# Optimization experiments

Hardware: AMD Instinct MI355X
Metric: run time of the kernel (lower is better)

The kernel has to match this reference:

```python
import jax, jax.numpy as jnp
import numpy as np

QB = 127.0  # 2**(8-1) - 1
LN_EPS = 1e-5


def _bitlinear(x, W):
    # LayerNorm (no affine)
    mu = jnp.mean(x, axis=-1, keepdims=True)
    var = jnp.mean((x - mu) ** 2, axis=-1, keepdims=True)
    xn = (x - mu) * jax.lax.rsqrt(var + LN_EPS)
    # per-tensor absmax activation fake-quant with STE
    eps = jnp.finfo(x.dtype).eps
    gamma = jnp.maximum(jnp.max(jnp.abs(xn)), 1e-8)
    xs = xn * (QB / gamma)
    xq_hard = jnp.round(jnp.clip(xs, -QB + eps, QB - eps))
    xq = xn + jax.lax.stop_gradient(xq_hard - xn)
    # binary weight quant: sign(W - mean(W)) with STE, scale beta = mean(|W|)
    alpha = jnp.mean(W)
    beta = jnp.maximum(jnp.mean(jnp.abs(W)), 1e-8)
    ws = W - alpha
    wb = ws + jax.lax.stop_gradient(jnp.where(ws > 0, 1.0, -1.0).astype(W.dtype) - ws)
    out = xq @ wb.T  # [B, out_features]
    return out * (beta * gamma / QB)


def setup_inputs() -> dict:
    key = jax.random.key(0)
    k0, k1, k2, k3 = jax.random.split(key, 4)
    B, D_IN, D_H, D_OUT = 131072, 256, 256, 256
    x = jax.random.normal(k0, (B, D_IN), dtype=jnp.float32)
    W1 = jax.random.normal(k1, (D_H, D_IN), dtype=jnp.float32) * 0.02
    W2 = jax.random.normal(k2, (D_H, D_H), dtype=jnp.float32) * 0.02
    W3 = jax.random.normal(k3, (D_OUT, D_H), dtype=jnp.float32) * 0.02
    return {"x": x, "W1": W1, "W2": W2, "W3": W3}


def reference(x, W1, W2, W3):
    h = jax.nn.relu(_bitlinear(x, W1))
    h = jax.nn.relu(_bitlinear(h, W2))
    return _bitlinear(h, W3)
```

## Files before the change

kernel.cpp:

```cpp
#include <hip/hip_runtime.h>
#include <stdint.h>

#define NROWS 131072
#define DIM 256

typedef __attribute__((ext_vector_type(4))) float f32x4;
typedef __attribute__((ext_vector_type(8))) float f32x8;
typedef __attribute__((ext_vector_type(8))) __bf16 bf16x8;
typedef __attribute__((ext_vector_type(8))) short s16x8;

__device__ __forceinline__ short bftrunc(float f) {
  return (short)(__float_as_uint(f) >> 16);
}

__global__ __launch_bounds__(256) void k_stats(const float* __restrict__ x,
                                               float* __restrict__ mu_o, float* __restrict__ rs_o,
                                               unsigned* __restrict__ gslot) {
  const int l = threadIdx.x & 63;
  const int gw = blockIdx.x * 4 + (threadIdx.x >> 6);
  float gmax = 0.f;
  for (int i = 0; i < 16; ++i) {
    const int row = gw * 16 + i;
    f32x4 v = *(const f32x4*)(x + (size_t)row * DIM + l * 4);
    float s = v.x + v.y + v.z + v.w;
    #pragma unroll
    for (int m = 1; m < 64; m <<= 1) s += __shfl_xor(s, m);
    const float mu = s * (1.f / 256.f);
    float d0 = v.x - mu, d1 = v.y - mu, d2 = v.z - mu, d3 = v.w - mu;
    float sq = d0 * d0 + d1 * d1 + d2 * d2 + d3 * d3;
    float am = fmaxf(fmaxf(fabsf(d0), fabsf(d1)), fmaxf(fabsf(d2), fabsf(d3)));
    #pragma unroll
    for (int m = 1; m < 64; m <<= 1) {
      sq += __shfl_xor(sq, m);
      am = fmaxf(am, __shfl_xor(am, m));
    }
    const float rstd = rsqrtf(sq * (1.f / 256.f) + 1e-5f);
    if (l == 0) { mu_o[row] = mu; rs_o[row] = rstd; }
    gmax = fmaxf(gmax, am * rstd);
  }
  if (l == 0) atomicMax(gslot + (gw & 63), __float_as_uint(gmax));
}

__global__ __launch_bounds__(256) void k_wstats1(const float* __restrict__ W0,
                                                 const float* __restrict__ W1,
                                                 const float* __restrict__ W2,
                                                 float2* __restrict__ part) {
  const int layer = blockIdx.y;
  const float* W = layer == 0 ? W0 : (layer == 1 ? W1 : W2);
  const int idx = (blockIdx.x * 256 + threadIdx.x) * 4;
  f32x4 v = *(const f32x4*)(W + idx);
  float s = v.x + v.y + v.z + v.w;
  float sa = fabsf(v.x) + fabsf(v.y) + fabsf(v.z) + fabsf(v.w);
  #pragma unroll
  for (int m = 1; m < 64; m <<= 1) { s += __shfl_xor(s, m); sa += __shfl_xor(sa, m); }
  __shared__ float bs[4], ba[4];
  const int w = threadIdx.x >> 6, l = threadIdx.x & 63;
  if (l == 0) { bs[w] = s; ba[w] = sa; }
  __syncthreads();
  if (threadIdx.x == 0) {
    float2 p;
    p.x = bs[0] + bs[1] + bs[2] + bs[3];
    p.y = ba[0] + ba[1] + ba[2] + ba[3];
    part[layer * 64 + blockIdx.x] = p;
  }
}

__global__ __launch_bounds__(64) void k_wstats2(const float2* __restrict__ part,
                                                float* __restrict__ ab) {
  const int layer = blockIdx.x;
  float2 p = part[layer * 64 + threadIdx.x];
  float s = p.x, sa = p.y;
  #pragma unroll
  for (int m = 1; m < 64; m <<= 1) { s += __shfl_xor(s, m); sa += __shfl_xor(sa, m); }
  if (threadIdx.x == 0) {
    ab[layer] = s * (1.f / 65536.f);
    ab[3 + layer] = fmaxf(sa * (1.f / 65536.f), 1e-8f);
  }
}

__global__ __launch_bounds__(256) void k_pack(const float* __restrict__ W0,
                                              const float* __restrict__ W1,
                                              const float* __restrict__ W2,
                                              const float* __restrict__ ab,
                                              unsigned short* __restrict__ bp) {
  const int layer = blockIdx.y;
  const float* W = layer == 0 ? W0 : (layer == 1 ? W1 : W2);
  const float alpha = ab[layer];
  const int p = blockIdx.x * 256 + threadIdx.x;
  const int r = p & 7, l = (p >> 3) & 63, nt = (p >> 9) & 15, kt = p >> 13;
  const int k = kt * 32 + ((l >> 4) << 3) + r;
  const int j = nt * 16 + (l & 15);
  const float wv = W[j * 256 + k] - alpha;
  bp[layer * 65536 + p] = (wv > 0.f) ? 0x3F80u : 0xBF80u;
}

template <int FINAL>
__global__ __launch_bounds__(256, 2) void k_gemm(
    const float* src, const float* __restrict__ mu, const float* __restrict__ rs,
    const unsigned* __restrict__ gslot, const unsigned short* __restrict__ bp,
    const float* __restrict__ beta_p,
    float* __restrict__ hout, float* bout,
    float* __restrict__ mu_n, float* __restrict__ rs_n, unsigned* __restrict__ gslot_n) {
  const int t = threadIdx.x, l = t & 63, w = t >> 6;
  const int row0 = blockIdx.x * 128 + w * 32;
  const int lr = l & 15, g2 = l >> 4;

  float gm = __uint_as_float(gslot[l]);
  #pragma unroll
  for (int m = 1; m < 64; m <<= 1) gm = fmaxf(gm, __shfl_xor(gm, m));
  const float gamma = fmaxf(gm, 1e-8f);
  const float qs = 127.f / gamma;
  const float beta = *beta_p;
  const float oscale = beta * gamma * (1.f / 127.f);

  const float mu0 = mu[row0 + lr],      rs0 = rs[row0 + lr];
  const float mu1 = mu[row0 + 16 + lr], rs1 = rs[row0 + 16 + lr];

  f32x4 acc[2][16];
  #pragma unroll
  for (int mt = 0; mt < 2; ++mt)
    #pragma unroll
    for (int i = 0; i < 16; ++i) acc[mt][i] = (f32x4){0.f, 0.f, 0.f, 0.f};

  const float* a0p = src + (size_t)(row0 + lr) * DIM + g2 * 8;
  const float* a1p = a0p + 16 * DIM;
  const unsigned short* bpl = bp + l * 8;

  #pragma unroll
  for (int c = 0; c < 8; ++c) {
    f32x8 v0 = *(const f32x8*)(a0p + c * 32);
    f32x8 v1 = *(const f32x8*)(a1p + c * 32);
    union { s16x8 s; bf16x8 b; } a0u, a1u;
    #pragma unroll
    for (int e = 0; e < 8; ++e) {
      float xn = (v0[e] - mu0) * rs0;
      float xs = xn * qs;
      xs = fminf(fmaxf(xs, -127.f), 127.f);
      a0u.s[e] = bftrunc(rintf(xs));
      float yn = (v1[e] - mu1) * rs1;
      float ys = yn * qs;
      ys = fminf(fmaxf(ys, -127.f), 127.f);
      a1u.s[e] = bftrunc(rintf(ys));
    }
    #pragma unroll
    for (int nt = 0; nt < 16; ++nt) {
      bf16x8 b = *(const bf16x8*)(bpl + (c * 16 + nt) * 512);
      acc[0][nt] = __builtin_amdgcn_mfma_f32_16x16x32_bf16(a0u.b, b, acc[0][nt], 0, 0, 0);
      acc[1][nt] = __builtin_amdgcn_mfma_f32_16x16x32_bf16(a1u.b, b, acc[1][nt], 0, 0, 0);
    }
  }

  if constexpr (FINAL == 1) {
    #pragma unroll
    for (int mt = 0; mt < 2; ++mt)
      #pragma unroll
      for (int nt = 0; nt < 16; ++nt)
        #pragma unroll
        for (int rr = 0; rr < 4; ++rr) {
          const int grow = row0 + mt * 16 + g2 * 4 + rr;
          bout[(size_t)grow * DIM + nt * 16 + lr] = acc[mt][nt][rr] * oscale;
        }
  } else {
    float gmax = 0.f;
    #pragma unroll
    for (int mt = 0; mt < 2; ++mt) {
      float sum[4] = {0.f, 0.f, 0.f, 0.f};
      #pragma unroll
      for (int nt = 0; nt < 16; ++nt)
        #pragma unroll
        for (int rr = 0; rr < 4; ++rr) {
          float h = fmaxf(acc[mt][nt][rr] * oscale, 0.f);
          acc[mt][nt][rr] = h;
          sum[rr] += h;
          hout[(size_t)(row0 + mt * 16 + g2 * 4 + rr) * DIM + nt * 16 + lr] = h;
        }
      #pragma unroll
      for (int rr = 0; rr < 4; ++rr) {
        float s_ = sum[rr];
        s_ += __shfl_xor(s_, 1); s_ += __shfl_xor(s_, 2);
        s_ += __shfl_xor(s_, 4); s_ += __shfl_xor(s_, 8);
        const float m_ = s_ * (1.f / 256.f);
        float sq = 0.f, am = 0.f;
        #pragma unroll
        for (int nt = 0; nt < 16; ++nt) {
          float d = acc[mt][nt][rr] - m_;
          sq += d * d;
          am = fmaxf(am, fabsf(d));
        }
        sq += __shfl_xor(sq, 1); sq += __shfl_xor(sq, 2);
        sq += __shfl_xor(sq, 4); sq += __shfl_xor(sq, 8);
        am = fmaxf(am, __shfl_xor(am, 1)); am = fmaxf(am, __shfl_xor(am, 2));
        am = fmaxf(am, __shfl_xor(am, 4)); am = fmaxf(am, __shfl_xor(am, 8));
        const float rstd = rsqrtf(sq * (1.f / 256.f) + 1e-5f);
        const int grow = row0 + mt * 16 + g2 * 4 + rr;
        if (lr == 0) { mu_n[grow] = m_; rs_n[grow] = rstd; }
        gmax = fmaxf(gmax, am * rstd);
      }
    }
    gmax = fmaxf(gmax, __shfl_xor(gmax, 16));
    gmax = fmaxf(gmax, __shfl_xor(gmax, 32));
    if (l == 0) atomicMax(gslot_n + (blockIdx.x & 63), __float_as_uint(gmax));
  }
}

extern "C" void kernel_launch(void* const* d_in, const int* in_sizes, int n_in,
                              void* d_out, int out_size, void* d_ws, size_t ws_size,
                              hipStream_t stream) {
  const float* x  = (const float*)d_in[0];
  const float* W1 = (const float*)d_in[1];
  const float* W2 = (const float*)d_in[2];
  const float* W3 = (const float*)d_in[3];

  char* ws = (char*)d_ws;
  unsigned* gslot = (unsigned*)ws;
  float* ab = (float*)(ws + 1024);
  float2* part = (float2*)(ws + 2048);
  float* muv = (float*)(ws + 4096);
  float* rsv = (float*)(ws + 4096 + 3 * 524288);
  unsigned short* bp = (unsigned short*)(ws + 3149824);
  float* h1 = (float*)(ws + 4194304);
  float* h2 = (float*)d_out;

  hipMemsetAsync(gslot, 0, 768, stream);
  dim3 wg(64, 3);
  k_wstats1<<<wg, 256, 0, stream>>>(W1, W2, W3, part);
  k_wstats2<<<3, 64, 0, stream>>>(part, ab);
  dim3 pg(256, 3);
  k_pack<<<pg, 256, 0, stream>>>(W1, W2, W3, ab, bp);
  k_stats<<<2048, 256, 0, stream>>>(x, muv, rsv, gslot);

  k_gemm<0><<<1024, 256, 0, stream>>>(x, muv, rsv, gslot, bp, ab + 3,
                                      h1, nullptr,
                                      muv + 131072, rsv + 131072, gslot + 64);
  k_gemm<0><<<1024, 256, 0, stream>>>(h1, muv + 131072, rsv + 131072, gslot + 64,
                                      bp + 65536, ab + 4,
                                      h2, nullptr,
                                      muv + 262144, rsv + 262144, gslot + 128);
  k_gemm<1><<<1024, 256, 0, stream>>>(h2, muv + 262144, rsv + 262144, gslot + 128,
                                      bp + 131072, ab + 5,
                                      nullptr, (float*)d_out,
                                      nullptr, nullptr, nullptr);
}
```

Before: 538.7 us.

## Stage A and B tiles through LDS with direct global-to-LDS loads

```diff
diff --git a/kernel.cpp b/kernel.cpp
--- a/kernel.cpp
+++ b/kernel.cpp
@@ -5,12 +5,23 @@
 #define DIM 256
 
 typedef __attribute__((ext_vector_type(4))) float f32x4;
-typedef __attribute__((ext_vector_type(8))) float f32x8;
 typedef __attribute__((ext_vector_type(8))) __bf16 bf16x8;
 typedef __attribute__((ext_vector_type(8))) short s16x8;
 
 __device__ __forceinline__ short bftrunc(float f) {
   return (short)(__float_as_uint(f) >> 16);
+}
+
+__device__ __forceinline__ short quant1(float v, float mu_, float rs_, float qs) {
+  float xn = (v - mu_) * rs_;
+  float xs = xn * qs;
+  xs = fminf(fmaxf(xs, -127.f), 127.f);
+  return bftrunc(rintf(xs));
+}
+
+__device__ __forceinline__ void gload_lds16(const void* g, void* lds) {
+  __builtin_amdgcn_global_load_lds((const __attribute__((address_space(1))) void*)g,
+                                   (__attribute__((address_space(3))) void*)lds, 16, 0, 0);
 }
 
 __global__ __launch_bounds__(256) void k_stats(const float* __restrict__ x,
@@ -95,15 +106,20 @@
 }
 
 template <int FINAL>
-__global__ __launch_bounds__(256, 2) void k_gemm(
+__global__ __launch_bounds__(256, 3) void k_gemm(
     const float* src, const float* __restrict__ mu, const float* __restrict__ rs,
     const unsigned* __restrict__ gslot, const unsigned short* __restrict__ bp,
     const float* __restrict__ beta_p,
     float* __restrict__ hout, float* bout,
     float* __restrict__ mu_n, float* __restrict__ rs_n, unsigned* __restrict__ gslot_n) {
+  __shared__ float Af[4096];
+  __shared__ unsigned short Bb[16384];
+  __shared__ float sS[2][64], sQ[2][64];
+
   const int t = threadIdx.x, l = t & 63, w = t >> 6;
-  const int row0 = blockIdx.x * 128 + w * 32;
   const int lr = l & 15, g2 = l >> 4;
+  const int wr = w >> 1, wc = w & 1;
+  const int row0 = blockIdx.x * 64;
 
   float gm = __uint_as_float(gslot[l]);
   #pragma unroll
@@ -113,92 +129,131 @@
   const float beta = *beta_p;
   const float oscale = beta * gamma * (1.f / 127.f);
 
-  const float mu0 = mu[row0 + lr],      rs0 = rs[row0 + lr];
-  const float mu1 = mu[row0 + 16 + lr], rs1 = rs[row0 + 16 + lr];
-
-  f32x4 acc[2][16];
+  const int arow = wr * 32 + lr;
+  const float mu0 = mu[row0 + arow],      rs0 = rs[row0 + arow];
+  const float mu1 = mu[row0 + arow + 16], rs1 = rs[row0 + arow + 16];
+
+  f32x4 acc[2][8];
   #pragma unroll
   for (int mt = 0; mt < 2; ++mt)
     #pragma unroll
-    for (int i = 0; i < 16; ++i) acc[mt][i] = (f32x4){0.f, 0.f, 0.f, 0.f};
-
-  const float* a0p = src + (size_t)(row0 + lr) * DIM + g2 * 8;
-  const float* a1p = a0p + 16 * DIM;
-  const unsigned short* bpl = bp + l * 8;
-
-  #pragma unroll
-  for (int c = 0; c < 8; ++c) {
-    f32x8 v0 = *(const f32x8*)(a0p + c * 32);
-    f32x8 v1 = *(const f32x8*)(a1p + c * 32);
-    union { s16x8 s; bf16x8 b; } a0u, a1u;
-    #pragma unroll
-    for (int e = 0; e < 8; ++e) {
-      float xn = (v0[e] - mu0) * rs0;
-      float xs = xn * qs;
-      xs = fminf(fmaxf(xs, -127.f), 127.f);
-      a0u.s[e] = bftrunc(rintf(xs));
-      float yn = (v1[e] - mu1) * rs1;
-      float ys = yn * qs;
-      ys = fminf(fmaxf(ys, -127.f), 127.f);
-      a1u.s[e] = bftrunc(rintf(ys));
-    }
-    #pragma unroll
-    for (int nt = 0; nt < 16; ++nt) {
-      bf16x8 b = *(const bf16x8*)(bpl + (c * 16 + nt) * 512);
-      acc[0][nt] = __builtin_amdgcn_mfma_f32_16x16x32_bf16(a0u.b, b, acc[0][nt], 0, 0, 0);
-      acc[1][nt] = __builtin_amdgcn_mfma_f32_16x16x32_bf16(a1u.b, b, acc[1][nt], 0, 0, 0);
-    }
+    for (int i = 0; i < 8; ++i) acc[mt][i] = (f32x4){0.f, 0.f, 0.f, 0.f};
+
+  for (int s = 0; s < 4; ++s) {
+    #pragma unroll
+    for (int it = 0; it < 4; ++it) {
+      const int d = w * 4096 + it * 1024 + l * 16;
+      const int row = d >> 8;
+      const int soff = (d & 255) ^ ((row & 7) << 4);
+      gload_lds16(src + (size_t)(row0 + row) * DIM + s * 64 + (soff >> 2),
+                  (char*)Af + d);
+    }
+    #pragma unroll
+    for (int it = 0; it < 8; ++it) {
+      const int d = w * 8192 + it * 1024 + l * 16;
+      gload_lds16(bp + s * 16384 + (d >> 1), (char*)Bb + d);
+    }
+    __syncthreads();
+
+    #pragma unroll
+    for (int kt2 = 0; kt2 < 2; ++kt2) {
+      bf16x8 af[2];
+      #pragma unroll
+      for (int mt = 0; mt < 2; ++mt) {
+        const int row = wr * 32 + mt * 16 + lr;
+        const int base = row * 256 + kt2 * 128 + g2 * 32;
+        const int sw = (lr & 7) << 4;
+        f32x4 v0 = *(const f32x4*)((const char*)Af + (base ^ sw));
+        f32x4 v1 = *(const f32x4*)((const char*)Af + ((base + 16) ^ sw));
+        const float mu_ = mt ? mu1 : mu0;
+        const float rs_ = mt ? rs1 : rs0;
+        union { s16x8 sv; bf16x8 bv; } u;
+        #pragma unroll
+        for (int e = 0; e < 4; ++e) {
+          u.sv[e]     = quant1(v0[e], mu_, rs_, qs);
+          u.sv[e + 4] = quant1(v1[e], mu_, rs_, qs);
+        }
+        af[mt] = u.bv;
+      }
+      #pragma unroll
+      for (int nt = 0; nt < 8; ++nt) {
+        const int ntg = wc * 8 + nt;
+        bf16x8 b = *(const bf16x8*)&Bb[((kt2 * 16 + ntg) * 64 + l) * 8];
+        acc[0][nt] = __builtin_amdgcn_mfma_f32_16x16x32_bf16(af[0], b, acc[0][nt], 0, 0, 0);
+        acc[1][nt] = __builtin_amdgcn_mfma_f32_16x16x32_bf16(af[1], b, acc[1][nt], 0, 0, 0);
+      }
+    }
+    __syncthreads();
   }
 
   if constexpr (FINAL == 1) {
     #pragma unroll
     for (int mt = 0; mt < 2; ++mt)
       #pragma unroll
-      for (int nt = 0; nt < 16; ++nt)
+      for (int nt = 0; nt < 8; ++nt)
         #pragma unroll
         for (int rr = 0; rr < 4; ++rr) {
-          const int grow = row0 + mt * 16 + g2 * 4 + rr;
-          bout[(size_t)grow * DIM + nt * 16 + lr] = acc[mt][nt][rr] * oscale;
+          const int grow = row0 + wr * 32 + mt * 16 + g2 * 4 + rr;
+          bout[(size_t)grow * DIM + (wc * 8 + nt) * 16 + lr] = acc[mt][nt][rr] * oscale;
         }
   } else {
-    float gmax = 0.f;
+    float ps[2][4], pq[2][4];
     #pragma unroll
     for (int mt = 0; mt < 2; ++mt) {
-      float sum[4] = {0.f, 0.f, 0.f, 0.f};
-      #pragma unroll
-      for (int nt = 0; nt < 16; ++nt)
+      #pragma unroll
+      for (int rr = 0; rr < 4; ++rr) { ps[mt][rr] = 0.f; pq[mt][rr] = 0.f; }
+      #pragma unroll
+      for (int nt = 0; nt < 8; ++nt)
         #pragma unroll
         for (int rr = 0; rr < 4; ++rr) {
           float h = fmaxf(acc[mt][nt][rr] * oscale, 0.f);
           acc[mt][nt][rr] = h;
-          sum[rr] += h;
-          hout[(size_t)(row0 + mt * 16 + g2 * 4 + rr) * DIM + nt * 16 + lr] = h;
+          ps[mt][rr] += h;
+          pq[mt][rr] += h * h;
+          hout[(size_t)(row0 + wr * 32 + mt * 16 + g2 * 4 + rr) * DIM + (wc * 8 + nt) * 16 + lr] = h;
         }
       #pragma unroll
       for (int rr = 0; rr < 4; ++rr) {
-        float s_ = sum[rr];
-        s_ += __shfl_xor(s_, 1); s_ += __shfl_xor(s_, 2);
-        s_ += __shfl_xor(s_, 4); s_ += __shfl_xor(s_, 8);
-        const float m_ = s_ * (1.f / 256.f);
-        float sq = 0.f, am = 0.f;
-        #pragma unroll
-        for (int nt = 0; nt < 16; ++nt) {
-          float d = acc[mt][nt][rr] - m_;
-          sq += d * d;
-          am = fmaxf(am, fabsf(d));
-        }
-        sq += __shfl_xor(sq, 1); sq += __shfl_xor(sq, 2);
-        sq += __shfl_xor(sq, 4); sq += __shfl_xor(sq, 8);
-        am = fmaxf(am, __shfl_xor(am, 1)); am = fmaxf(am, __shfl_xor(am, 2));
-        am = fmaxf(am, __shfl_xor(am, 4)); am = fmaxf(am, __shfl_xor(am, 8));
-        const float rstd = rsqrtf(sq * (1.f / 256.f) + 1e-5f);
-        const int grow = row0 + mt * 16 + g2 * 4 + rr;
-        if (lr == 0) { mu_n[grow] = m_; rs_n[grow] = rstd; }
+        #pragma unroll
+        for (int m = 1; m < 16; m <<= 1) {
+          ps[mt][rr] += __shfl_xor(ps[mt][rr], m);
+          pq[mt][rr] += __shfl_xor(pq[mt][rr], m);
+        }
+      }
+    }
+    if (lr == 0) {
+      #pragma unroll
+      for (int mt = 0; mt < 2; ++mt)
+        #pragma unroll
+        for (int rr = 0; rr < 4; ++rr) {
+          const int row_l = wr * 32 + mt * 16 + g2 * 4 + rr;
+          sS[wc][row_l] = ps[mt][rr];
+          sQ[wc][row_l] = pq[mt][rr];
+        }
+    }
+    __syncthreads();
+    float gmax = 0.f;
+    #pragma unroll
+    for (int mt = 0; mt < 2; ++mt)
+      #pragma unroll
+      for (int rr = 0; rr < 4; ++rr) {
+        const int row_l = wr * 32 + mt * 16 + g2 * 4 + rr;
+        const float s_all = sS[0][row_l] + sS[1][row_l];
+        const float q_all = sQ[0][row_l] + sQ[1][row_l];
+        const float m_ = s_all * (1.f / 256.f);
+        const float var = q_all * (1.f / 256.f) - m_ * m_;
+        const float rstd = rsqrtf(var + 1e-5f);
+        if (wc == 0 && lr == 0) {
+          mu_n[row0 + row_l] = m_;
+          rs_n[row0 + row_l] = rstd;
+        }
+        float am = 0.f;
+        #pragma unroll
+        for (int nt = 0; nt < 8; ++nt) am = fmaxf(am, fabsf(acc[mt][nt][rr] - m_));
         gmax = fmaxf(gmax, am * rstd);
       }
-    }
-    gmax = fmaxf(gmax, __shfl_xor(gmax, 16));
-    gmax = fmaxf(gmax, __shfl_xor(gmax, 32));
+    #pragma unroll
+    for (int m = 1; m < 64; m <<= 1) gmax = fmaxf(gmax, __shfl_xor(gmax, m));
     if (l == 0) atomicMax(gslot_n + (blockIdx.x & 63), __float_as_uint(gmax));
   }
 }
@@ -229,14 +284,14 @@
   k_pack<<<pg, 256, 0, stream>>>(W1, W2, W3, ab, bp);
   k_stats<<<2048, 256, 0, stream>>>(x, muv, rsv, gslot);
 
-  k_gemm<0><<<1024, 256, 0, stream>>>(x, muv, rsv, gslot, bp, ab + 3,
+  k_gemm<0><<<2048, 256, 0, stream>>>(x, muv, rsv, gslot, bp, ab + 3,
                                       h1, nullptr,
                                       muv + 131072, rsv + 131072, gslot + 64);
-  k_gemm<0><<<1024, 256, 0, stream>>>(h1, muv + 131072, rsv + 131072, gslot + 64,
+  k_gemm<0><<<2048, 256, 0, stream>>>(h1, muv + 131072, rsv + 131072, gslot + 64,
                                       bp + 65536, ab + 4,
                                       h2, nullptr,
                                       muv + 262144, rsv + 262144, gslot + 128);
-  k_gemm<1><<<1024, 256, 0, stream>>>(h2, muv + 262144, rsv + 262144, gslot + 128,
+  k_gemm<1><<<2048, 256, 0, stream>>>(h2, muv + 262144, rsv + 262144, gslot + 128,
                                       bp + 131072, ab + 5,
                                       nullptr, (float*)d_out,
                                       nullptr, nullptr, nullptr);
```

New measurement: 444.0 us. -17.6%, faster.
